# Kernel tuning notes

Measured on AMD Instinct MI355X. Metric: run time of the kernel, lower is better.

Reference implementation:

```python
import jax, jax.numpy as jnp
import numpy as np

EPS = 1e-10  # faithful quirk: masked scores are set to eps, NOT -inf
LN_EPS = 1e-5
N_HEADS, D_MODEL, D_HEAD, D_MLP = 16, 1024, 64, 4096
INIT_RANGE = 0.02


def setup_inputs() -> dict:
    key = jax.random.key(0)
    ks = jax.random.split(key, 8)
    B, S = 2, 2048
    inp = {
        'residual': jax.random.normal(ks[0], (B, S, D_MODEL), jnp.float32),
        'W_key': jax.random.normal(ks[1], (N_HEADS, D_MODEL, D_HEAD), jnp.float32) * INIT_RANGE,
        'W_query': jax.random.normal(ks[2], (N_HEADS, D_MODEL, D_HEAD), jnp.float32) * INIT_RANGE,
        'W_values': jax.random.normal(ks[3], (N_HEADS, D_MODEL, D_HEAD), jnp.float32) * INIT_RANGE,
        'W_attn_out': jax.random.normal(ks[4], (N_HEADS, D_HEAD, D_MODEL), jnp.float32) * INIT_RANGE,
        'B_key': jnp.zeros((N_HEADS, D_HEAD), jnp.float32),
        'B_query': jnp.zeros((N_HEADS, D_HEAD), jnp.float32),
        'B_values': jnp.zeros((N_HEADS, D_HEAD), jnp.float32),
        'B_attn_out': jnp.zeros((D_MODEL,), jnp.float32),
        'ln1_w': jnp.ones((D_MODEL,), jnp.float32),
        'ln1_b': jnp.zeros((D_MODEL,), jnp.float32),
        'ln2_w': jnp.ones((D_MODEL,), jnp.float32),
        'ln2_b': jnp.zeros((D_MODEL,), jnp.float32),
        'W_mlp_in': jax.random.normal(ks[5], (D_MODEL, D_MLP), jnp.float32) * INIT_RANGE,
        'W_mlp_out': jax.random.normal(ks[6], (D_MLP, D_MODEL), jnp.float32) * INIT_RANGE,
        'B_mlp_in': jnp.zeros((D_MLP,), jnp.float32),
        'B_mlp_out': jnp.zeros((D_MODEL,), jnp.float32),
    }
    return inp


def _layernorm(x, w, b):
    mean = jnp.mean(x, axis=-1, keepdims=True)
    var = jnp.mean(jnp.square(x - mean), axis=-1, keepdims=True)  # biased var
    return (x - mean) / jnp.sqrt(var + LN_EPS) * w + b


def _attention(x, W_key, W_query, W_values, W_attn_out,
               B_key, B_query, B_values, B_attn_out):
    S = x.shape[1]
    keys = jnp.einsum('bse,neh->bsnh', x, W_key) + B_key
    queries = jnp.einsum('bse,neh->bsnh', x, W_query) + B_query
    values = jnp.einsum('bse,neh->bsnh', x, W_values) + B_values
    scores = jnp.einsum('bknh,bqnh->bnqk', keys, queries) / (D_HEAD ** 0.5)
    # faithful to source: positions where query < key are set to eps (not -inf)
    q_idx = jnp.arange(S)[:, None]
    k_idx = jnp.arange(S)[None, :]
    scores = jnp.where(q_idx < k_idx, EPS, scores)
    probs = jax.nn.softmax(scores, axis=3)
    weighted = jnp.einsum('bnqk,bknh->bqnh', probs, values)
    out = jnp.einsum('bqnh,nhe->bqe', weighted, W_attn_out) + B_attn_out
    return out


def reference(residual, W_key, W_query, W_values, W_attn_out,
              B_key, B_query, B_values, B_attn_out,
              ln1_w, ln1_b, ln2_w, ln2_b,
              W_mlp_in, W_mlp_out, B_mlp_in, B_mlp_out):
    mid = _attention(_layernorm(residual, ln1_w, ln1_b),
                     W_key, W_query, W_values, W_attn_out,
                     B_key, B_query, B_values, B_attn_out) + residual
    h = jnp.einsum('bse,em->bsm', _layernorm(mid, ln2_w, ln2_b), W_mlp_in) + B_mlp_in
    h = jax.nn.gelu(h, approximate=False)  # torch nn.GELU default = exact erf
    out = jnp.einsum('bsm,me->bse', h, W_mlp_out) + B_mlp_out + mid
    return out
```

## Files before the change

kernel.cpp:

```cpp
#include <hip/hip_runtime.h>
#include <hip/hip_bf16.h>


typedef __hip_bfloat16 bf16;
typedef __bf16 bf16x8 __attribute__((ext_vector_type(8)));
typedef float f32x4 __attribute__((ext_vector_type(4)));
typedef unsigned short u16x8 __attribute__((ext_vector_type(8)));
#define DEV static __device__ __forceinline__

DEV float b2f(bf16 v) { return __bfloat162float(v); }
DEV bf16 f2b(float v) { return __float2bfloat16(v); }
DEV unsigned short f2bu(float v) { return __builtin_bit_cast(unsigned short, __float2bfloat16(v)); }
DEV float ldin(const void* p, size_t i, int f32) {
  return f32 ? ((const float*)p)[i] : b2f(((const bf16*)p)[i]);
}
DEV void stout(void* p, size_t i, int f32, float v) {
  if (f32) ((float*)p)[i] = v;
  else     ((bf16*)p)[i] = f2b(v);
}
DEV f32x4 mfma16(bf16x8 a, bf16x8 b, f32x4 c) {
  return __builtin_amdgcn_mfma_f32_16x16x32_bf16(a, b, c, 0, 0, 0);
}
DEV float exp2fast(float x) {
  float r;
  asm volatile("v_exp_f32 %0, %1\n\ts_nop 0" : "=v"(r) : "v"(x));
  return r;
}
DEV void gload16(const void* g, void* l) {
  __builtin_amdgcn_global_load_lds(
      (const __attribute__((address_space(1))) unsigned int*)g,
      (__attribute__((address_space(3))) unsigned int*)l, 16, 0, 0);
}

__global__ void detect_kernel(const void* __restrict__ ln1w, int* __restrict__ flag) {
  if (threadIdx.x == 0 && blockIdx.x == 0) {
    const unsigned short* u = (const unsigned short*)ln1w;
    flag[0] = (u[0] == 0x3F80u) ? 0 : 1;
  }
}

__global__ void pack_bias(const void* __restrict__ Bq, const void* __restrict__ Bk,
                          const void* __restrict__ Bv, const void* __restrict__ Bao,
                          const void* __restrict__ Bmi, const void* __restrict__ Bmo,
                          const int* __restrict__ flagp, float* __restrict__ out) {
  int t = blockIdx.x * 256 + threadIdx.x;
  if (t >= 9216) return;
  int f32 = flagp[0];
  float v;
  if (t < 1024)      v = ldin(Bq, t, f32);
  else if (t < 2048) v = ldin(Bk, t - 1024, f32);
  else if (t < 3072) v = ldin(Bv, t - 2048, f32);
  else if (t < 4096) v = ldin(Bao, t - 3072, f32);
  else if (t < 8192) v = ldin(Bmi, t - 4096, f32);
  else               v = ldin(Bmo, t - 8192, f32);
  out[t] = v;
}

__global__ __launch_bounds__(256) void tsplit(const void* __restrict__ src,
                                              bf16* __restrict__ hi,
                                              const int* __restrict__ flagp,
                                              int K, int N) {
  int i = blockIdx.x * 256 + threadIdx.x;
  int f32 = flagp[0];
  int k = i / N, n = i - k * N;
  float v = ldin(src, i, f32);
  hi[(size_t)n * K + k] = f2b(v);
}

__global__ __launch_bounds__(256) void tsplit_qkv(const void* __restrict__ Wq,
                                                  const void* __restrict__ Wk,
                                                  const void* __restrict__ Wv,
                                                  bf16* __restrict__ hi,
                                                  const int* __restrict__ flagp) {
  int i = blockIdx.x * 256 + threadIdx.x;
  int f32 = flagp[0];
  int sec = i >> 20;
  int rem = i & 1048575;
  int hh = rem >> 16, kr = rem & 65535;
  int k = kr >> 6, d = kr & 63;
  const void* W = (sec == 0) ? Wq : (sec == 1) ? Wk : Wv;
  float v = ldin(W, (size_t)hh * 65536 + (size_t)k * 64 + d, f32);
  int n = sec * 1024 + hh * 64 + d;
  hi[(size_t)n * 1024 + k] = f2b(v);
}

__global__ __launch_bounds__(256) void vsuffix(const bf16* __restrict__ v2,
                                               float* __restrict__ suf) {
  const int head = blockIdx.x >> 6, d = blockIdx.x & 63;
  const int t = threadIdx.x;
  const int T = t >> 3, s0 = (t & 7) * 8;
  const bf16* src = v2 + (size_t)head * 131072 + (size_t)T * 4096 + d * 64 + s0;
  u16x8 u = *(const u16x8*)src;
  float s = 0.f;
#pragma unroll
  for (int j = 0; j < 8; j++) s += b2f(__builtin_bit_cast(bf16, (unsigned short)u[j]));
#pragma unroll
  for (int off = 1; off < 8; off <<= 1) s += __shfl_xor(s, off);
  __shared__ float cs[32];
  if ((t & 7) == 0) cs[T] = s;
  __syncthreads();
  if (t < 33) {
    float acc = 0.f;
    for (int j = t; j < 32; j++) acc += cs[j];
    suf[((size_t)head * 33 + t) * 64 + d] = acc;
  }
}

__global__ __launch_bounds__(256) void ln_kernel(const void* __restrict__ x,
                                                 const void* __restrict__ w,
                                                 const void* __restrict__ bb,
                                                 bf16* __restrict__ out,
                                                 const int* __restrict__ flagp) {
  const int f32 = flagp[0];
  const int row = blockIdx.x, t = threadIdx.x;
  const size_t base = (size_t)row * 1024;
  float v[4];
#pragma unroll
  for (int i = 0; i < 4; i++) v[i] = ldin(x, base + t + 256 * i, f32);
  float s1 = v[0] + v[1] + v[2] + v[3];
  float s2 = v[0] * v[0] + v[1] * v[1] + v[2] * v[2] + v[3] * v[3];
#pragma unroll
  for (int off = 32; off; off >>= 1) {
    s1 += __shfl_xor(s1, off);
    s2 += __shfl_xor(s2, off);
  }
  __shared__ float r1[4], r2[4];
  if ((t & 63) == 0) { r1[t >> 6] = s1; r2[t >> 6] = s2; }
  __syncthreads();
  s1 = r1[0] + r1[1] + r1[2] + r1[3];
  s2 = r2[0] + r2[1] + r2[2] + r2[3];
  float mean = s1 * (1.f / 1024.f);
  float var = s2 * (1.f / 1024.f) - mean * mean;
  float rstd = rsqrtf(var + 1e-5f);
#pragma unroll
  for (int i = 0; i < 4; i++) {
    int idx = t + 256 * i;
    out[base + idx] = f2b((v[i] - mean) * rstd * ldin(w, idx, f32) + ldin(bb, idx, f32));
  }
}

template <int MODE>
__global__ __launch_bounds__(256) void gemm_bt2(const bf16* __restrict__ A,
                                                const bf16* __restrict__ BT,
                                                const float* __restrict__ bias,
                                                const void* extra, void* outp,
                                                const int* __restrict__ flagp,
                                                int N, int K) {
  __shared__ __align__(16) unsigned short As[128][64];
  __shared__ __align__(16) unsigned short Bs[128][64];
  const int f32 = flagp[0];
  const int t = threadIdx.x;
  const int lane = t & 63, wv = t >> 6;
  const int quad = lane >> 4, l15 = lane & 15;
  const int wm = (wv >> 1) * 64, wn = (wv & 1) * 64;
  const int m0 = blockIdx.y * 128, n0 = blockIdx.x * 128;
  f32x4 acc[4][4] = {};
  const int rl = lane >> 3, G = lane & 7;
  const int sg = (G ^ rl) * 8;
  const int l7 = l15 & 7;
  for (int k0 = 0; k0 < K; k0 += 64) {
#pragma unroll
    for (int c = 0; c < 4; c++) {
      const int ch = wv * 4 + c;
      const int row = ch * 8 + rl;
      gload16(A + (size_t)(m0 + row) * K + k0 + sg, &As[ch * 8][0]);
      gload16(BT + (size_t)(n0 + row) * K + k0 + sg, &Bs[ch * 8][0]);
    }
    __syncthreads();
#pragma unroll
    for (int sub = 0; sub < 2; sub++) {
      const int gsw = (((sub * 4 + quad) ^ l7)) * 8;
      bf16x8 af[4], bh[4];
#pragma unroll
      for (int f = 0; f < 4; f++) {
        af[f] = __builtin_bit_cast(bf16x8, *(const u16x8*)&As[wm + f * 16 + l15][gsw]);
        bh[f] = __builtin_bit_cast(bf16x8, *(const u16x8*)&Bs[wn + f * 16 + l15][gsw]);
      }
#pragma unroll
      for (int fm = 0; fm < 4; fm++)
#pragma unroll
        for (int fn = 0; fn < 4; fn++)
          acc[fm][fn] = mfma16(af[fm], bh[fn], acc[fm][fn]);
    }
    __syncthreads();
  }
  if (MODE == 3) {
    bf16* q2 = (bf16*)outp;
    bf16* k2 = q2 + 4194304;
    bf16* v2 = (bf16*)const_cast<void*>(extra);
#pragma unroll
    for (int fm = 0; fm < 4; fm++) {
      int rowb = m0 + wm + fm * 16 + quad * 4;
      int bq = rowb >> 11, sb = rowb & 2047;
#pragma unroll
      for (int fn = 0; fn < 4; fn++) {
        int col = n0 + wn + fn * 16 + l15;
        float bcol = bias[col];
        int sec = col >> 10;
        int hd = col & 1023;
        size_t hbase = (size_t)(bq * 16 + (hd >> 6)) * 131072;
        int d = hd & 63;
        if (sec == 2) {
          unsigned long long pk = 0;
#pragma unroll
          for (int r = 0; r < 4; r++)
            pk |= (unsigned long long)f2bu(acc[fm][fn][r] + bcol) << (16 * r);
          *(unsigned long long*)&v2[hbase + (size_t)(sb >> 6) * 4096 + d * 64 + (sb & 63)] = pk;
        } else {
          bf16* dst = sec ? k2 : q2;
#pragma unroll
          for (int r = 0; r < 4; r++)
            dst[hbase + (size_t)(sb + r) * 64 + d] = f2b(acc[fm][fn][r] + bcol);
        }
      }
    }
  } else {
#pragma unroll
    for (int fm = 0; fm < 4; fm++) {
#pragma unroll
      for (int r = 0; r < 4; r++) {
        int row = m0 + wm + fm * 16 + quad * 4 + r;
#pragma unroll
        for (int fn = 0; fn < 4; fn++) {
          int col = n0 + wn + fn * 16 + l15;
          float v = acc[fm][fn][r] + bias[col];
          if (MODE == 1) {
            size_t idx = (size_t)row * N + col;
            v += ldin(extra, idx, f32);
            stout(outp, idx, f32, v);
          } else {
            v = 0.5f * v * (1.f + erff(v * 0.70710678118654752f));
            ((bf16*)outp)[(size_t)row * N + col] = f2b(v);
          }
        }
      }
    }
  }
}

__global__ __launch_bounds__(256) void gemm_bt3(const bf16* __restrict__ A,
                                                const bf16* __restrict__ BT,
                                                const float* __restrict__ bias,
                                                const void* extra, void* outp,
                                                const int* __restrict__ flagp,
                                                int N, int K) {
  __shared__ __align__(16) unsigned short As[64][64];
  __shared__ __align__(16) unsigned short Bs[128][64];
  const int f32 = flagp[0];
  const int t = threadIdx.x;
  const int lane = t & 63, wv = t >> 6;
  const int quad = lane >> 4, l15 = lane & 15;
  const int wm = (wv >> 1) * 32, wn = (wv & 1) * 64;
  const int m0 = blockIdx.y * 64, n0 = blockIdx.x * 128;
  f32x4 acc[2][4] = {};
  const int rl = lane >> 3, G = lane & 7;
  const int sg = (G ^ rl) * 8;
  const int l7 = l15 & 7;
  for (int k0 = 0; k0 < K; k0 += 64) {
#pragma unroll
    for (int c = 0; c < 2; c++) {
      const int ch = wv * 2 + c;
      gload16(A + (size_t)(m0 + ch * 8 + rl) * K + k0 + sg, &As[ch * 8][0]);
    }
#pragma unroll
    for (int c = 0; c < 4; c++) {
      const int ch = wv * 4 + c;
      gload16(BT + (size_t)(n0 + ch * 8 + rl) * K + k0 + sg, &Bs[ch * 8][0]);
    }
    __syncthreads();
#pragma unroll
    for (int sub = 0; sub < 2; sub++) {
      const int gsw = (((sub * 4 + quad) ^ l7)) * 8;
      bf16x8 af[2], bh[4];
#pragma unroll
      for (int f = 0; f < 2; f++)
        af[f] = __builtin_bit_cast(bf16x8, *(const u16x8*)&As[wm + f * 16 + l15][gsw]);
#pragma unroll
      for (int f = 0; f < 4; f++)
        bh[f] = __builtin_bit_cast(bf16x8, *(const u16x8*)&Bs[wn + f * 16 + l15][gsw]);
#pragma unroll
      for (int fm = 0; fm < 2; fm++)
#pragma unroll
        for (int fn = 0; fn < 4; fn++)
          acc[fm][fn] = mfma16(af[fm], bh[fn], acc[fm][fn]);
    }
    __syncthreads();
  }
#pragma unroll
  for (int fm = 0; fm < 2; fm++) {
#pragma unroll
    for (int r = 0; r < 4; r++) {
      int row = m0 + wm + fm * 16 + quad * 4 + r;
#pragma unroll
      for (int fn = 0; fn < 4; fn++) {
        int col = n0 + wn + fn * 16 + l15;
        float v = acc[fm][fn][r] + bias[col];
        size_t idx = (size_t)row * N + col;
        v += ldin(extra, idx, f32);
        stout(outp, idx, f32, v);
      }
    }
  }
}

template <int MODE, int QKV>
__global__ __launch_bounds__(256) void gemm_nn(const bf16* __restrict__ A,
                                               const void* __restrict__ B0,
                                               const void* __restrict__ B1,
                                               const void* __restrict__ B2,
                                               const float* __restrict__ bias,
                                               const void* extra, void* outp,
                                               const int* __restrict__ flagp,
                                               int N, int K, size_t ooff) {
  __shared__ unsigned short As[128][40];
  __shared__ unsigned short Bh[128][40];
  __shared__ unsigned short Bl[128][40];
  const int f32 = flagp[0];
  const int t = threadIdx.x;
  const int lane = t & 63, wv = t >> 6;
  const int quad = lane >> 4, l15 = lane & 15;
  const int wm = (wv >> 1) * 64, wn = (wv & 1) * 64;
  const int m0 = blockIdx.y * 128, n0 = blockIdx.x * 128;
  const void* B = B0;
  if (QKV) B = (n0 < 1024) ? B0 : (n0 < 2048) ? B1 : B2;
  f32x4 acc[4][4] = {};
  const int row_a = t >> 2;
  const int kc = (t & 3) * 8;
  const int cB = t & 127;
  const int e0 = t >> 7;
  for (int k0 = 0; k0 < K; k0 += 32) {
    uint4 a0 = *(const uint4*)(A + (size_t)(m0 + row_a) * K + k0 + kc);
    uint4 a1 = *(const uint4*)(A + (size_t)(m0 + 64 + row_a) * K + k0 + kc);
    *(uint4*)&As[row_a][kc] = a0;
    *(uint4*)&As[64 + row_a][kc] = a1;
#pragma unroll
    for (int rep = 0; rep < 8; rep++) {
      int e = (rep * 2 + e0) * 2;
      size_t a0i, a1i;
      if (QKV) {
        int cs = (n0 + cB) & 1023;
        size_t wb = (size_t)(cs >> 6) * 65536 + (cs & 63);
        a0i = wb + (size_t)(k0 + e) * 64;
        a1i = wb + (size_t)(k0 + e + 1) * 64;
      } else {
        a0i = (size_t)(k0 + e) * N + n0 + cB;
        a1i = a0i + N;
      }
      float v0 = ldin(B, a0i, f32);
      float v1 = ldin(B, a1i, f32);
      unsigned short h0 = f2bu(v0), h1 = f2bu(v1);
      float l0 = v0 - b2f(__builtin_bit_cast(bf16, h0));
      float l1 = v1 - b2f(__builtin_bit_cast(bf16, h1));
      *(unsigned int*)&Bh[cB][e] = (unsigned int)h0 | ((unsigned int)h1 << 16);
      *(unsigned int*)&Bl[cB][e] = (unsigned int)f2bu(l0) | ((unsigned int)f2bu(l1) << 16);
    }
    __syncthreads();
    bf16x8 af[4], bh[4], bl[4];
#pragma unroll
    for (int f = 0; f < 4; f++) {
      af[f] = __builtin_bit_cast(bf16x8, *(const u16x8*)&As[wm + f * 16 + l15][quad * 8]);
      bh[f] = __builtin_bit_cast(bf16x8, *(const u16x8*)&Bh[wn + f * 16 + l15][quad * 8]);
      bl[f] = __builtin_bit_cast(bf16x8, *(const u16x8*)&Bl[wn + f * 16 + l15][quad * 8]);
    }
#pragma unroll
    for (int fm = 0; fm < 4; fm++)
#pragma unroll
      for (int fn = 0; fn < 4; fn++)
        acc[fm][fn] = mfma16(af[fm], bh[fn], acc[fm][fn]);
    if (f32) {
#pragma unroll
      for (int fm = 0; fm < 4; fm++)
#pragma unroll
        for (int fn = 0; fn < 4; fn++)
          acc[fm][fn] = mfma16(af[fm], bl[fn], acc[fm][fn]);
    }
    __syncthreads();
  }
#pragma unroll
  for (int fm = 0; fm < 4; fm++) {
#pragma unroll
    for (int r = 0; r < 4; r++) {
      int row = m0 + wm + fm * 16 + quad * 4 + r;
#pragma unroll
      for (int fn = 0; fn < 4; fn++) {
        int col = n0 + wn + fn * 16 + l15;
        float v = acc[fm][fn][r] + bias[col];
        size_t idx = (size_t)row * N + col;
        if (MODE == 1) {
          v += ldin(extra, ooff + idx, f32);
          stout(outp, ooff + idx, f32, v);
        } else if (MODE == 2) {
          v = 0.5f * v * (1.f + erff(v * 0.70710678118654752f));
          ((bf16*)outp)[idx] = f2b(v);
        } else {
          ((bf16*)outp)[idx] = f2b(v);
        }
      }
    }
  }
}

__global__ __launch_bounds__(256, 2) void attn_split(const bf16* __restrict__ qkv2,
                                                     const float* __restrict__ suf,
                                                     float* __restrict__ part0,
                                                     float* __restrict__ part1,
                                                     float* __restrict__ lp0buf,
                                                     float* __restrict__ lp1buf,
                                                     bf16* __restrict__ weighted) {
  __shared__ __align__(16) unsigned short P[4][4][16][72];
  const int t = threadIdx.x;
  const int lane = t & 63, wv = t >> 6;
  const int quad = lane >> 4, l15 = lane & 15;
  const int w = blockIdx.x * 4 + wv;
  const int g = w & 31;
  const int wi = w >> 5;
  int qc, Tlo, Thi, mode;
  if (wi < 32) {
    qc = 31 - (wi >> 1);
    if ((wi & 1) == 0) { Tlo = 0; Thi = 15; mode = 1; }
    else               { Tlo = 16; Thi = qc; mode = 2; }
  } else {
    qc = 47 - wi; Tlo = 0; Thi = qc; mode = 0;
  }
  const int b = g >> 4, n = g & 15;
  const bf16* Qh = qkv2 + (size_t)g * 131072;
  const bf16* Kh = qkv2 + 4194304 + (size_t)g * 131072;
  const bf16* Vh = qkv2 + 8388608 + (size_t)g * 131072;
  bf16x8 aq[4][2];
#pragma unroll
  for (int qg = 0; qg < 4; qg++) {
    size_t qr = (size_t)(qc * 64 + qg * 16 + l15) * 64;
    aq[qg][0] = __builtin_bit_cast(bf16x8, *(const u16x8*)(Qh + qr + quad * 8));
    aq[qg][1] = __builtin_bit_cast(bf16x8, *(const u16x8*)(Qh + qr + 32 + quad * 8));
  }
  float lp[4][4] = {};
  f32x4 o[4][4] = {};
  const float C = 0.125f * 1.44269504088896f;
  for (int T = Tlo; T <= Thi; ++T) {
    const int kk = T * 64;
    u16x8 uk[4][2];
#pragma unroll
    for (int sub = 0; sub < 4; sub++) {
      size_t kr = (size_t)(kk + sub * 16 + l15) * 64;
      uk[sub][0] = *(const u16x8*)(Kh + kr + quad * 8);
      uk[sub][1] = *(const u16x8*)(Kh + kr + 32 + quad * 8);
    }
    const bf16* Vt = Vh + (size_t)T * 4096;
    u16x8 vu[2][4];
#pragma unroll
    for (int sl = 0; sl < 2; sl++)
#pragma unroll
      for (int f = 0; f < 4; f++)
        vu[sl][f] = *(const u16x8*)(Vt + (size_t)(f * 16 + l15) * 64 + sl * 32 + quad * 8);
#pragma unroll
    for (int qg = 0; qg < 4; qg++) {
      const int qgb = qc * 64 + qg * 16 + quad * 4;
      f32x4 s[4];
#pragma unroll
      for (int sub = 0; sub < 4; sub++) {
        f32x4 sc = {0.f, 0.f, 0.f, 0.f};
        sc = mfma16(aq[qg][0], __builtin_bit_cast(bf16x8, uk[sub][0]), sc);
        sc = mfma16(aq[qg][1], __builtin_bit_cast(bf16x8, uk[sub][1]), sc);
        s[sub] = sc;
      }
#pragma unroll
      for (int sub = 0; sub < 4; sub++) {
#pragma unroll
        for (int r = 0; r < 4; r++) {
          float pv = exp2fast(s[sub][r] * C);
          int kg = kk + sub * 16 + l15;
          pv = (qgb + r < kg) ? 1.0f : pv;
          lp[qg][r] += pv;
          P[wv][qg][quad * 4 + r][l15 + 16 * sub] = f2bu(pv);
        }
      }
      u16x8 pu0 = *(const u16x8*)&P[wv][qg][l15][quad * 8];
      u16x8 pu1 = *(const u16x8*)&P[wv][qg][l15][32 + quad * 8];
#pragma unroll
      for (int f = 0; f < 4; f++) {
        o[qg][f] = mfma16(__builtin_bit_cast(bf16x8, pu0), __builtin_bit_cast(bf16x8, vu[0][f]), o[qg][f]);
        o[qg][f] = mfma16(__builtin_bit_cast(bf16x8, pu1), __builtin_bit_cast(bf16x8, vu[1][f]), o[qg][f]);
      }
    }
  }
  if (mode != 1) {
    const float* sp = suf + ((size_t)g * 33 + (qc + 1)) * 64;
#pragma unroll
    for (int f = 0; f < 4; f++) {
      float sv = sp[f * 16 + l15];
#pragma unroll
      for (int qg = 0; qg < 4; qg++)
#pragma unroll
        for (int r = 0; r < 4; r++) o[qg][f][r] += sv;
    }
  }
#pragma unroll
  for (int off = 8; off; off >>= 1)
#pragma unroll
    for (int qg = 0; qg < 4; qg++)
#pragma unroll
      for (int r = 0; r < 4; r++) lp[qg][r] += __shfl_xor(lp[qg][r], off);
  if (mode == 0) {
    const float mcnt = (float)(2048 - 64 * (qc + 1));
#pragma unroll
    for (int qg = 0; qg < 4; qg++) {
#pragma unroll
      for (int r = 0; r < 4; r++) {
        float inv = 1.f / (lp[qg][r] + mcnt);
        int qg_row = qc * 64 + qg * 16 + quad * 4 + r;
        size_t base = (size_t)(b * 2048 + qg_row) * 1024 + n * 64;
#pragma unroll
        for (int f = 0; f < 4; f++)
          weighted[base + f * 16 + l15] = f2b(o[qg][f][r] * inv);
      }
    }
  } else {
    float* part = (mode == 1) ? part0 : part1;
    float* lpb  = (mode == 1) ? lp0buf : lp1buf;
    size_t pb = (size_t)(g * 16 + (qc - 16)) * 4096;
#pragma unroll
    for (int qg = 0; qg < 4; qg++) {
#pragma unroll
      for (int r = 0; r < 4; r++) {
        int row = qg * 16 + quad * 4 + r;
#pragma unroll
        for (int f = 0; f < 4; f++)
          part[pb + (size_t)row * 64 + f * 16 + l15] = o[qg][f][r];
        if (l15 == 0) lpb[(size_t)(g * 16 + (qc - 16)) * 64 + row] = lp[qg][r];
      }
    }
  }
}

__global__ __launch_bounds__(256) void attn_combine(const float* __restrict__ part0,
                                                    const float* __restrict__ part1,
                                                    const float* __restrict__ lp0,
                                                    const float* __restrict__ lp1,
                                                    bf16* __restrict__ weighted) {
  int i = blockIdx.x * 256 + threadIdx.x;
  int d = i & 63, row = (i >> 6) & 63, qq = (i >> 12) & 15, g = i >> 16;
  int qc = qq + 16;
  size_t pi = ((size_t)(g * 16 + qq) * 64 + row) * 64 + d;
  float o = part0[pi] + part1[pi];
  size_t li = (size_t)(g * 16 + qq) * 64 + row;
  float mcnt = (float)(2048 - 64 * (qc + 1));
  float lp = lp0[li] + lp1[li] + mcnt;
  int b = g >> 4, n = g & 15;
  int qg = qc * 64 + row;
  weighted[(size_t)(b * 2048 + qg) * 1024 + n * 64 + d] = f2b(o / lp);
}

__global__ __launch_bounds__(256) void attn_old(const bf16* __restrict__ qkv,
                                                bf16* __restrict__ weighted) {
  __shared__ unsigned short P[4][16][40];
  const int t = threadIdx.x;
  const int lane = t & 63, wv = t >> 6;
  const int quad = lane >> 4, l15 = lane & 15;
  const int bid = blockIdx.x;
  const int qc = bid & 31, bn = bid >> 5;
  const int b = bn >> 4, n = bn & 15;
  const int q0 = qc * 64 + wv * 16;
  const bf16* Qb = qkv + (size_t)b * 2048 * 3072 + n * 64;
  const bf16* Kb = Qb + 1024;
  const unsigned short* Vus = (const unsigned short*)(Qb + 2048);
  bf16x8 aq0, aq1;
  {
    u16x8 u0 = *(const u16x8*)(Qb + (size_t)(q0 + l15) * 3072 + quad * 8);
    u16x8 u1 = *(const u16x8*)(Qb + (size_t)(q0 + l15) * 3072 + 32 + quad * 8);
    aq0 = __builtin_bit_cast(bf16x8, u0);
    aq1 = __builtin_bit_cast(bf16x8, u1);
  }
  float m_[4] = {-30000.f, -30000.f, -30000.f, -30000.f};
  float l_[4] = {0.f, 0.f, 0.f, 0.f};
  f32x4 o[4] = {};
  for (int kk = 0; kk < 2048; kk += 32) {
    f32x4 s[2];
#pragma unroll
    for (int sub = 0; sub < 2; sub++) {
      int krow = kk + sub * 16 + l15;
      u16x8 uk0 = *(const u16x8*)(Kb + (size_t)krow * 3072 + quad * 8);
      u16x8 uk1 = *(const u16x8*)(Kb + (size_t)krow * 3072 + 32 + quad * 8);
      f32x4 sc = {0.f, 0.f, 0.f, 0.f};
      sc = mfma16(aq0, __builtin_bit_cast(bf16x8, uk0), sc);
      sc = mfma16(aq1, __builtin_bit_cast(bf16x8, uk1), sc);
#pragma unroll
      for (int r = 0; r < 4; r++) {
        int qg = q0 + quad * 4 + r;
        int kg = kk + sub * 16 + l15;
        s[sub][r] = (qg < kg) ? 1e-10f : sc[r] * 0.125f;
      }
    }
    float mr[4];
#pragma unroll
    for (int r = 0; r < 4; r++) mr[r] = fmaxf(s[0][r], s[1][r]);
#pragma unroll
    for (int off = 8; off; off >>= 1)
#pragma unroll
      for (int r = 0; r < 4; r++) mr[r] = fmaxf(mr[r], __shfl_xor(mr[r], off));
    float al[4];
#pragma unroll
    for (int r = 0; r < 4; r++) {
      float mn = fmaxf(m_[r], mr[r]);
      al[r] = __expf(m_[r] - mn);
      m_[r] = mn;
    }
    f32x4 p0, p1;
    float rs[4];
#pragma unroll
    for (int r = 0; r < 4; r++) {
      p0[r] = __expf(s[0][r] - m_[r]);
      p1[r] = __expf(s[1][r] - m_[r]);
      rs[r] = p0[r] + p1[r];
    }
#pragma unroll
    for (int off = 8; off; off >>= 1)
#pragma unroll
      for (int r = 0; r < 4; r++) rs[r] += __shfl_xor(rs[r], off);
#pragma unroll
    for (int r = 0; r < 4; r++) l_[r] = l_[r] * al[r] + rs[r];
#pragma unroll
    for (int f = 0; f < 4; f++)
#pragma unroll
      for (int r = 0; r < 4; r++) o[f][r] *= al[r];
#pragma unroll
    for (int r = 0; r < 4; r++) {
      P[wv][quad * 4 + r][l15] = f2bu(p0[r]);
      P[wv][quad * 4 + r][16 + l15] = f2bu(p1[r]);
    }
    __syncthreads();
    u16x8 pu = *(const u16x8*)&P[wv][l15][quad * 8];
    bf16x8 pf = __builtin_bit_cast(bf16x8, pu);
#pragma unroll
    for (int f = 0; f < 4; f++) {
      u16x8 vu;
#pragma unroll
      for (int j = 0; j < 8; j++)
        vu[j] = Vus[(size_t)(kk + quad * 8 + j) * 3072 + f * 16 + l15];
      o[f] = mfma16(pf, __builtin_bit_cast(bf16x8, vu), o[f]);
    }
    __syncthreads();
  }
#pragma unroll
  for (int r = 0; r < 4; r++) {
    float inv = 1.f / l_[r];
    int qg = q0 + quad * 4 + r;
    size_t base = (size_t)(b * 2048 + qg) * 1024 + n * 64;
#pragma unroll
    for (int f = 0; f < 4; f++)
      weighted[base + f * 16 + l15] = f2b(o[f][r] * inv);
  }
}

extern "C" void kernel_launch(void* const* d_in, const int* in_sizes, int n_in,
                              void* d_out, int out_size, void* d_ws, size_t ws_size,
                              hipStream_t stream) {
  const void* residual = d_in[0];
  const void* W_key    = d_in[1];
  const void* W_query  = d_in[2];
  const void* W_values = d_in[3];
  const void* W_ao     = d_in[4];
  const void* B_key    = d_in[5];
  const void* B_query  = d_in[6];
  const void* B_values = d_in[7];
  const void* B_ao     = d_in[8];
  const void* ln1w     = d_in[9];
  const void* ln1b     = d_in[10];
  const void* ln2w     = d_in[11];
  const void* ln2b     = d_in[12];
  const void* W_mi     = d_in[13];
  const void* W_mo     = d_in[14];
  const void* B_mi     = d_in[15];
  const void* B_mo     = d_in[16];

  char* ws = (char*)d_ws;
  float* biasA  = (float*)ws;
  int*   flag   = (int*)(ws + 36864);
  bf16*  slotA  = (bf16*)(ws + 40960);
  bf16*  xn = slotA, *wtd = slotA, *xn2 = slotA;

  detect_kernel<<<1, 64, 0, stream>>>(ln1w, flag);
  pack_bias<<<36, 256, 0, stream>>>(B_query, B_key, B_values, B_ao, B_mi, B_mo,
                                    flag, biasA);

  if (ws_size >= (size_t)83927040) {
    bf16*  qkv2    = (bf16*)(ws + 8429568);
    bf16*  q2      = qkv2;
    bf16*  v2      = qkv2 + 8388608;
    bf16*  h       = (bf16*)(ws + 8429568);
    bf16*  qkvT_hi = (bf16*)(ws + 33595392);
    float* suf     = (float*)(ws + 39886848);
    float* lp0buf  = (float*)(ws + 40157184);
    float* lp1buf  = (float*)(ws + 40288256);
    bf16*  aoT_hi  = (bf16*)(ws + 46178304);
    bf16*  miT_hi  = (bf16*)(ws + 50372608);
    float* part0   = (float*)(ws + 58761216);
    bf16*  moT_hi  = (bf16*)(ws + 67149824);
    float* part1   = (float*)(ws + 75538432);

    tsplit_qkv<<<12288, 256, 0, stream>>>(W_query, W_key, W_values, qkvT_hi, flag);
    tsplit<<<4096, 256, 0, stream>>>(W_ao, aoT_hi, flag, 1024, 1024);
    tsplit<<<16384, 256, 0, stream>>>(W_mi, miT_hi, flag, 1024, 4096);
    tsplit<<<16384, 256, 0, stream>>>(W_mo, moT_hi, flag, 4096, 1024);

    ln_kernel<<<4096, 256, 0, stream>>>(residual, ln1w, ln1b, xn, flag);
    gemm_bt2<3><<<dim3(24, 32), 256, 0, stream>>>(xn, qkvT_hi, biasA,
                                                  v2, q2, flag, 3072, 1024);
    vsuffix<<<2048, 256, 0, stream>>>(v2, suf);
    attn_split<<<384, 256, 0, stream>>>(qkv2, suf, part0, part1,
                                        lp0buf, lp1buf, wtd);
    attn_combine<<<8192, 256, 0, stream>>>(part0, part1, lp0buf, lp1buf, wtd);
    gemm_bt3<<<dim3(8, 64), 256, 0, stream>>>(wtd, aoT_hi, biasA + 3072,
                                              residual, d_out, flag, 1024, 1024);
    ln_kernel<<<4096, 256, 0, stream>>>(d_out, ln2w, ln2b, xn2, flag);
    gemm_bt2<2><<<dim3(32, 32), 256, 0, stream>>>(xn2, miT_hi, biasA + 4096,
                                                  nullptr, h, flag, 4096, 1024);
    gemm_bt3<<<dim3(8, 64), 256, 0, stream>>>(h, moT_hi, biasA + 8192,
                                              d_out, d_out, flag, 1024, 4096);
  } else {
    bf16* qkv   = (bf16*)(ws + 8429568);
    bf16* hhalf = (bf16*)(ws + 16818176);

    ln_kernel<<<4096, 256, 0, stream>>>(residual, ln1w, ln1b, xn, flag);
    gemm_nn<0, 1><<<dim3(24, 32), 256, 0, stream>>>(xn, W_query, W_key, W_values,
                                                    biasA, nullptr, qkv, flag,
                                                    3072, 1024, 0);
    attn_old<<<1024, 256, 0, stream>>>(qkv, wtd);
    gemm_nn<1, 0><<<dim3(8, 32), 256, 0, stream>>>(wtd, W_ao, nullptr, nullptr,
                                                   biasA + 3072, residual, d_out,
                                                   flag, 1024, 1024, 0);
    ln_kernel<<<4096, 256, 0, stream>>>(d_out, ln2w, ln2b, xn2, flag);
    for (int half = 0; half < 2; ++half) {
      const bf16* a2 = xn2 + (size_t)half * 2048 * 1024;
      size_t ooff = (size_t)half * 2048 * 1024;
      gemm_nn<2, 0><<<dim3(32, 16), 256, 0, stream>>>(a2, W_mi, nullptr, nullptr,
                                                      biasA + 4096, nullptr, hhalf,
                                                      flag, 4096, 1024, 0);
      gemm_nn<1, 0><<<dim3(8, 16), 256, 0, stream>>>(hhalf, W_mo, nullptr, nullptr,
                                                     biasA + 8192, d_out, d_out,
                                                     flag, 1024, 4096, ooff);
    }
  }
}
```

Measured before the change: 465.3 us.

## Remap GEMM blocks across XCDs and double-buffer K loads in attention

The GEMM kernels now launch a 1D grid and permute block IDs so that consecutive tiles land on the same XCD (blockIdx mod 8), which is meant to improve L2 reuse of A/B tiles. The attention kernel's K-tile loads are double-buffered, so the next tile's K fragments are fetched while the current tile computes. It also raises wave priority around the MFMA sections with s_setprio. The extra K buffer raises register pressure, and the ID remap assumes the grid size is a multiple of 8.

After: 561.4 us. 1.21x slower.

```diff
diff --git a/kernel.cpp b/kernel.cpp
--- a/kernel.cpp
+++ b/kernel.cpp
@@ -145,7 +145,7 @@
                                                 const float* __restrict__ bias,
                                                 const void* extra, void* outp,
                                                 const int* __restrict__ flagp,
-                                                int N, int K) {
+                                                int N, int K, int nx) {
   __shared__ __align__(16) unsigned short As[128][64];
   __shared__ __align__(16) unsigned short Bs[128][64];
   const int f32 = flagp[0];
@@ -153,7 +153,9 @@
   const int lane = t & 63, wv = t >> 6;
   const int quad = lane >> 4, l15 = lane & 15;
   const int wm = (wv >> 1) * 64, wn = (wv & 1) * 64;
-  const int m0 = blockIdx.y * 128, n0 = blockIdx.x * 128;
+  const int pB = blockIdx.x, cpx = gridDim.x >> 3;
+  const int id = (pB & 7) * cpx + (pB >> 3);
+  const int m0 = (id / nx) * 128, n0 = (id % nx) * 128;
   f32x4 acc[4][4] = {};
   const int rl = lane >> 3, G = lane & 7;
   const int sg = (G ^ rl) * 8;
@@ -251,7 +253,9 @@
   const int lane = t & 63, wv = t >> 6;
   const int quad = lane >> 4, l15 = lane & 15;
   const int wm = (wv >> 1) * 32, wn = (wv & 1) * 64;
-  const int m0 = blockIdx.y * 64, n0 = blockIdx.x * 128;
+  const int pB = blockIdx.x, cpx = gridDim.x >> 3;
+  const int id = (pB & 7) * cpx + (pB >> 3);
+  const int m0 = (id >> 3) * 64, n0 = (id & 7) * 128;
   f32x4 acc[2][4] = {};
   const int rl = lane >> 3, G = lane & 7;
   const int sg = (G ^ rl) * 8;
@@ -436,15 +440,17 @@
   float lp[4][4] = {};
   f32x4 o[4][4] = {};
   const float C = 0.125f * 1.44269504088896f;
-  for (int T = Tlo; T <= Thi; ++T) {
+  auto loadK = [&](int T, u16x8 (&uk)[4][2]) {
     const int kk = T * 64;
-    u16x8 uk[4][2];
 #pragma unroll
     for (int sub = 0; sub < 4; sub++) {
       size_t kr = (size_t)(kk + sub * 16 + l15) * 64;
       uk[sub][0] = *(const u16x8*)(Kh + kr + quad * 8);
       uk[sub][1] = *(const u16x8*)(Kh + kr + 32 + quad * 8);
     }
+  };
+  auto computeT = [&](int T, u16x8 (&uk)[4][2]) {
+    const int kk = T * 64;
     const bf16* Vt = Vh + (size_t)T * 4096;
     u16x8 vu[2][4];
 #pragma unroll
@@ -456,6 +462,7 @@
     for (int qg = 0; qg < 4; qg++) {
       const int qgb = qc * 64 + qg * 16 + quad * 4;
       f32x4 s[4];
+      __builtin_amdgcn_s_setprio(1);
 #pragma unroll
       for (int sub = 0; sub < 4; sub++) {
         f32x4 sc = {0.f, 0.f, 0.f, 0.f};
@@ -463,6 +470,7 @@
         sc = mfma16(aq[qg][1], __builtin_bit_cast(bf16x8, uk[sub][1]), sc);
         s[sub] = sc;
       }
+      __builtin_amdgcn_s_setprio(0);
 #pragma unroll
       for (int sub = 0; sub < 4; sub++) {
 #pragma unroll
@@ -476,13 +484,25 @@
       }
       u16x8 pu0 = *(const u16x8*)&P[wv][qg][l15][quad * 8];
       u16x8 pu1 = *(const u16x8*)&P[wv][qg][l15][32 + quad * 8];
+      __builtin_amdgcn_s_setprio(1);
 #pragma unroll
       for (int f = 0; f < 4; f++) {
         o[qg][f] = mfma16(__builtin_bit_cast(bf16x8, pu0), __builtin_bit_cast(bf16x8, vu[0][f]), o[qg][f]);
         o[qg][f] = mfma16(__builtin_bit_cast(bf16x8, pu1), __builtin_bit_cast(bf16x8, vu[1][f]), o[qg][f]);
       }
-    }
-  }
+      __builtin_amdgcn_s_setprio(0);
+    }
+  };
+  u16x8 ukA[4][2], ukB[4][2];
+  loadK(Tlo, ukA);
+  int T = Tlo;
+  for (; T + 1 <= Thi; T += 2) {
+    loadK(T + 1, ukB);
+    computeT(T, ukA);
+    if (T + 2 <= Thi) loadK(T + 2, ukA);
+    computeT(T + 1, ukB);
+  }
+  if (T <= Thi) computeT(T, ukA);
   if (mode != 1) {
     const float* sp = suf + ((size_t)g * 33 + (qc + 1)) * 64;
 #pragma unroll
@@ -703,19 +723,19 @@
     tsplit<<<16384, 256, 0, stream>>>(W_mo, moT_hi, flag, 4096, 1024);
 
     ln_kernel<<<4096, 256, 0, stream>>>(residual, ln1w, ln1b, xn, flag);
-    gemm_bt2<3><<<dim3(24, 32), 256, 0, stream>>>(xn, qkvT_hi, biasA,
-                                                  v2, q2, flag, 3072, 1024);
+    gemm_bt2<3><<<768, 256, 0, stream>>>(xn, qkvT_hi, biasA,
+                                         v2, q2, flag, 3072, 1024, 24);
     vsuffix<<<2048, 256, 0, stream>>>(v2, suf);
     attn_split<<<384, 256, 0, stream>>>(qkv2, suf, part0, part1,
                                         lp0buf, lp1buf, wtd);
     attn_combine<<<8192, 256, 0, stream>>>(part0, part1, lp0buf, lp1buf, wtd);
-    gemm_bt3<<<dim3(8, 64), 256, 0, stream>>>(wtd, aoT_hi, biasA + 3072,
-                                              residual, d_out, flag, 1024, 1024);
+    gemm_bt3<<<512, 256, 0, stream>>>(wtd, aoT_hi, biasA + 3072,
+                                      residual, d_out, flag, 1024, 1024);
     ln_kernel<<<4096, 256, 0, stream>>>(d_out, ln2w, ln2b, xn2, flag);
-    gemm_bt2<2><<<dim3(32, 32), 256, 0, stream>>>(xn2, miT_hi, biasA + 4096,
-                                                  nullptr, h, flag, 4096, 1024);
-    gemm_bt3<<<dim3(8, 64), 256, 0, stream>>>(h, moT_hi, biasA + 8192,
-                                              d_out, d_out, flag, 1024, 4096);
+    gemm_bt2<2><<<1024, 256, 0, stream>>>(xn2, miT_hi, biasA + 4096,
+                                          nullptr, h, flag, 4096, 1024, 32);
+    gemm_bt3<<<512, 256, 0, stream>>>(h, moT_hi, biasA + 8192,
+                                      d_out, d_out, flag, 1024, 4096);
   } else {
     bf16* qkv   = (bf16*)(ws + 8429568);
     bf16* hhalf = (bf16*)(ws + 16818176);
```
